# Kernel tuning notes

Hardware: AMD Instinct MI355X
Metric: run time of the kernel (lower is better)

## Reference

```python
import jax, jax.numpy as jnp
import numpy as np
from jax import lax

CHAOS_R = 3.5699456
N_STEPS = 10


def setup_inputs() -> dict:
    key = jax.random.key(0)
    k1, k2, k3 = jax.random.split(key, 3)
    B, T, D = 256, 8192, 5
    x = jax.random.normal(k1, (B, T, D), dtype=jnp.float32)
    temple = jax.random.normal(k2, (4, 5), dtype=jnp.float32)
    breath_vector = jax.random.normal(k3, (5,), dtype=jnp.float32)
    return {"x": x, "temple": temple, "breath_vector": breath_vector}


def reference(x, temple, breath_vector):
    # x: (B, T, D) with D == 5
    B, T, D = x.shape

    # mirror_sequence: chaos logistic map on mean of x[0,0]
    seed = jnp.mod(jnp.mean(x[0, 0]), 1.0)
    chaos = CHAOS_R * seed * (1.0 - seed)
    mirrored = jnp.where(chaos > 0.7, 9.0 - x,
                         jnp.where(chaos > 0.4, jnp.flip(x, axis=1), x))
    mode_code = jnp.where(chaos > 0.7, 0, jnp.where(chaos > 0.4, 1, 2))  # 0=invert,1=retrograde,2=none

    extended_x = jnp.concatenate([x, mirrored], axis=1)  # (B, 2T, D)

    # per-token breath: first T tokens use breath[:4], mirrored half uses breath[1:5]
    breath_main = breath_vector[:4]
    breath_mirror = breath_vector[1:5]
    breath = jnp.concatenate([
        jnp.broadcast_to(breath_main, (T, 4)),
        jnp.broadcast_to(breath_mirror, (T, 4)),
    ], axis=0)  # (2T, 4)

    def step(vec, _):
        # vec: (B, 2T, 5)
        transformed = jnp.einsum('rd,btd->btr', temple, vec)  # (B, 2T, 4)
        resonance = jnp.sum(transformed * breath[None, :, :], axis=-1)  # (B, 2T)
        vec = jnp.roll(vec, shift=1, axis=-1).at[..., 0].set(jnp.mod(resonance, 10.0))
        return vec, resonance

    vec0 = extended_x[..., :5]
    _, history = lax.scan(step, vec0, None, length=N_STEPS)  # (10, B, 2T)

    # torch.std default is unbiased (ddof=1)
    score = 1.0 / (1.0 + jnp.std(history, axis=0, ddof=1))  # (B, 2T)
    gate_weights = score[..., None]  # (B, 2T, 1)
    return gate_weights, extended_x, mode_code
```

## Files before the change

### kernel.cpp

```cpp
#include <hip/hip_runtime.h>

#define B_DIM 256
#define T_DIM 8192
#define D_DIM 5
#define NSTEPS 10

static constexpr long long GATE_N = (long long)B_DIM * (2 * T_DIM);
static constexpr long long EXT_N  = GATE_N * D_DIM;

__device__ __forceinline__ float scan_score(double v0, double v1, double v2, double v3, double v4,
                                            double w0, double w1, double w2, double w3, double w4) {
    float h[NSTEPS];
#pragma unroll
    for (int s = 0; s < NSTEPS; ++s) {
        double res = v0 * w0;
        res = fma(v1, w1, res);
        res = fma(v2, w2, res);
        res = fma(v3, w3, res);
        res = fma(v4, w4, res);
        h[s] = (float)res;
        double q = floor(res * 0.1);
        double m = fma(q, -10.0, res);
        m = (m < 0.0)   ? m + 10.0 : m;
        m = (m >= 10.0) ? m - 10.0 : m;
        v4 = v3; v3 = v2; v2 = v1; v1 = v0; v0 = m;
    }
    float mean = 0.f;
#pragma unroll
    for (int s = 0; s < NSTEPS; ++s) mean += h[s];
    mean *= 0.1f;
    float ssd = 0.f;
#pragma unroll
    for (int s = 0; s < NSTEPS; ++s) { float d = h[s] - mean; ssd = fmaf(d, d, ssd); }
    float sd = sqrtf(ssd * (1.0f / 9.0f));
    return 1.0f / (1.0f + sd);
}

__global__ __launch_bounds__(256) void temple_gate_kernel(
    const float* __restrict__ x, const float* __restrict__ temple,
    const float* __restrict__ breath, float* __restrict__ out) {
    __shared__ double sw[10];
    __shared__ int s_mode;

    if (threadIdx.x == 0) {
        double s = 0.0;
        for (int d = 0; d < 5; ++d) s += (double)x[d];
        s = s / 5.0;
        double seed = s - floor(s);
        double chaos = 3.5699456 * seed * (1.0 - seed);
        int mode = (chaos > 0.7) ? 0 : ((chaos > 0.4) ? 1 : 2);
        s_mode = mode;
        for (int d = 0; d < 5; ++d) {
            double wm = 0.0, wx = 0.0;
            for (int r = 0; r < 4; ++r) {
                double tv = (double)temple[r * 5 + d];
                wm += (double)breath[r] * tv;
                wx += (double)breath[r + 1] * tv;
            }
            sw[d] = wm; sw[5 + d] = wx;
        }
        if (blockIdx.x == 0) out[GATE_N + EXT_N] = (float)mode;
    }
    __syncthreads();

    const int mode = s_mode;
    const double wm0 = sw[0], wm1 = sw[1], wm2 = sw[2], wm3 = sw[3], wm4 = sw[4];
    const double wx0 = sw[5], wx1 = sw[6], wx2 = sw[7], wx3 = sw[8], wx4 = sw[9];

    const long long tid = (long long)blockIdx.x * blockDim.x + threadIdx.x;
    const int b = (int)(tid >> 13);
    const int t = (int)(tid & (T_DIM - 1));

    const float* xp = x + ((long long)b * T_DIM + t) * D_DIM;
    const float x0 = xp[0], x1 = xp[1], x2 = xp[2], x3 = xp[3], x4 = xp[4];

    float* gate = out;
    float* ext  = out + GATE_N;
    const long long rowBase = (long long)b * (2 * T_DIM);

    {
        const long long o = (rowBase + t) * D_DIM;
        ext[o + 0] = x0; ext[o + 1] = x1; ext[o + 2] = x2; ext[o + 3] = x3; ext[o + 4] = x4;
        gate[rowBase + t] = scan_score((double)x0, (double)x1, (double)x2, (double)x3, (double)x4,
                                       wm0, wm1, wm2, wm3, wm4);
    }

    {
        double m0 = (double)x0, m1 = (double)x1, m2 = (double)x2, m3 = (double)x3, m4 = (double)x4;
        float  f0 = x0, f1 = x1, f2 = x2, f3 = x3, f4 = x4;
        if (mode == 0) {
            m0 = 9.0 - m0; m1 = 9.0 - m1; m2 = 9.0 - m2; m3 = 9.0 - m3; m4 = 9.0 - m4;
            f0 = 9.f - x0; f1 = 9.f - x1; f2 = 9.f - x2; f3 = 9.f - x3; f4 = 9.f - x4;
        }
        const int tm = (mode == 1) ? (T_DIM - 1 - t) : t;
        const long long p = rowBase + T_DIM + tm;
        const long long o = p * D_DIM;
        ext[o + 0] = f0; ext[o + 1] = f1; ext[o + 2] = f2; ext[o + 3] = f3; ext[o + 4] = f4;
        gate[p] = scan_score(m0, m1, m2, m3, m4, wx0, wx1, wx2, wx3, wx4);
    }
}

extern "C" void kernel_launch(void* const* d_in, const int* in_sizes, int n_in,
                              void* d_out, int out_size, void* d_ws, size_t ws_size,
                              hipStream_t stream) {
    const float* x      = (const float*)d_in[0];
    const float* temple = (const float*)d_in[1];
    const float* breath = (const float*)d_in[2];
    float* out = (float*)d_out;

    const int total = B_DIM * T_DIM;
    temple_gate_kernel<<<total / 256, 256, 0, stream>>>(x, temple, breath, out);
}
```

Measured before the change: 145.1 us.

## Tile tokens through LDS with float4 coalesced loads and stores

Each block now handles a 1024-token tile. It loads the x tile with coalesced float4 reads into LDS, writes the extended output with float4 stores, and handles the retrograde case by reading the tile reversed from LDS. Each thread computes four tokens' scores and writes the gates as float4. The per-block mode and weight setup is now computed redundantly by every thread instead of once through shared memory. The aim is to replace the strided 5-float accesses with wide coalesced transfers, at the cost of fewer blocks and more work per thread.

After: 145.4 us. About the same (+0.2%).

```diff
diff --git a/kernel.cpp b/kernel.cpp
--- a/kernel.cpp
+++ b/kernel.cpp
@@ -1,23 +1,22 @@
 #include <hip/hip_runtime.h>
 
-#define B_DIM 256
-#define T_DIM 8192
-#define D_DIM 5
 #define NSTEPS 10
-
-static constexpr long long GATE_N = (long long)B_DIM * (2 * T_DIM);
-static constexpr long long EXT_N  = GATE_N * D_DIM;
+constexpr int B_DIM = 256, T_DIM = 8192, D_DIM = 5;
+constexpr int TILE  = 1024;
+constexpr int BLOCK = 256;
+constexpr long long GATE_N = (long long)B_DIM * 2 * T_DIM;
+constexpr long long EXT_N  = GATE_N * D_DIM;
 
 __device__ __forceinline__ float scan_score(double v0, double v1, double v2, double v3, double v4,
-                                            double w0, double w1, double w2, double w3, double w4) {
+                                            const double* __restrict__ w) {
     float h[NSTEPS];
 #pragma unroll
     for (int s = 0; s < NSTEPS; ++s) {
-        double res = v0 * w0;
-        res = fma(v1, w1, res);
-        res = fma(v2, w2, res);
-        res = fma(v3, w3, res);
-        res = fma(v4, w4, res);
+        double res = v0 * w[0];
+        res = fma(v1, w[1], res);
+        res = fma(v2, w[2], res);
+        res = fma(v3, w[3], res);
+        res = fma(v4, w[4], res);
         h[s] = (float)res;
         double q = floor(res * 0.1);
         double m = fma(q, -10.0, res);
@@ -36,67 +35,101 @@
     return 1.0f / (1.0f + sd);
 }
 
-__global__ __launch_bounds__(256) void temple_gate_kernel(
+__global__ __launch_bounds__(BLOCK) void temple_gate_kernel(
     const float* __restrict__ x, const float* __restrict__ temple,
     const float* __restrict__ breath, float* __restrict__ out) {
-    __shared__ double sw[10];
-    __shared__ int s_mode;
+    __shared__ float lds[TILE * D_DIM];
 
-    if (threadIdx.x == 0) {
-        double s = 0.0;
-        for (int d = 0; d < 5; ++d) s += (double)x[d];
-        s = s / 5.0;
-        double seed = s - floor(s);
-        double chaos = 3.5699456 * seed * (1.0 - seed);
-        int mode = (chaos > 0.7) ? 0 : ((chaos > 0.4) ? 1 : 2);
-        s_mode = mode;
-        for (int d = 0; d < 5; ++d) {
-            double wm = 0.0, wx = 0.0;
-            for (int r = 0; r < 4; ++r) {
-                double tv = (double)temple[r * 5 + d];
-                wm += (double)breath[r] * tv;
-                wx += (double)breath[r + 1] * tv;
-            }
-            sw[d] = wm; sw[5 + d] = wx;
+    const int k  = threadIdx.x;
+    const int b  = blockIdx.x >> 3;
+    const int t0 = (blockIdx.x & 7) * TILE;
+
+    double s = 0.0;
+    for (int d = 0; d < 5; ++d) s += (double)x[d];
+    s = s / 5.0;
+    double seed  = s - floor(s);
+    double chaos = 3.5699456 * seed * (1.0 - seed);
+    const int mode = (chaos > 0.7) ? 0 : ((chaos > 0.4) ? 1 : 2);
+    double wm[5], wx[5];
+#pragma unroll
+    for (int d = 0; d < 5; ++d) {
+        double a = 0.0, c = 0.0;
+#pragma unroll
+        for (int r = 0; r < 4; ++r) {
+            double tv = (double)temple[r * 5 + d];
+            a += (double)breath[r]     * tv;
+            c += (double)breath[r + 1] * tv;
         }
-        if (blockIdx.x == 0) out[GATE_N + EXT_N] = (float)mode;
+        wm[d] = a; wx[d] = c;
     }
-    __syncthreads();
+    if (blockIdx.x == 0 && k == 0) out[GATE_N + EXT_N] = (float)mode;
 
-    const int mode = s_mode;
-    const double wm0 = sw[0], wm1 = sw[1], wm2 = sw[2], wm3 = sw[3], wm4 = sw[4];
-    const double wx0 = sw[5], wx1 = sw[6], wx2 = sw[7], wx3 = sw[8], wx4 = sw[9];
+    const long long srcBase = ((long long)b * T_DIM + t0) * D_DIM;
+    const float4* __restrict__ src = (const float4*)(x + srcBase);
+    float4 r0 = src[k],       r1 = src[k + 256], r2 = src[k + 512],
+           r3 = src[k + 768], r4 = src[k + 1024];
 
-    const long long tid = (long long)blockIdx.x * blockDim.x + threadIdx.x;
-    const int b = (int)(tid >> 13);
-    const int t = (int)(tid & (T_DIM - 1));
-
-    const float* xp = x + ((long long)b * T_DIM + t) * D_DIM;
-    const float x0 = xp[0], x1 = xp[1], x2 = xp[2], x3 = xp[3], x4 = xp[4];
+    float4* l4 = (float4*)lds;
+    l4[k] = r0; l4[k + 256] = r1; l4[k + 512] = r2; l4[k + 768] = r3; l4[k + 1024] = r4;
 
     float* gate = out;
     float* ext  = out + GATE_N;
     const long long rowBase = (long long)b * (2 * T_DIM);
 
     {
-        const long long o = (rowBase + t) * D_DIM;
-        ext[o + 0] = x0; ext[o + 1] = x1; ext[o + 2] = x2; ext[o + 3] = x3; ext[o + 4] = x4;
-        gate[rowBase + t] = scan_score((double)x0, (double)x1, (double)x2, (double)x3, (double)x4,
-                                       wm0, wm1, wm2, wm3, wm4);
+        float4* dst = (float4*)(ext + (rowBase + t0) * D_DIM);
+        dst[k] = r0; dst[k + 256] = r1; dst[k + 512] = r2; dst[k + 768] = r3; dst[k + 1024] = r4;
+    }
+    if (mode == 0) {
+        float4* dst = (float4*)(ext + (rowBase + T_DIM + t0) * D_DIM);
+        float4 m0 = make_float4(9.f - r0.x, 9.f - r0.y, 9.f - r0.z, 9.f - r0.w);
+        float4 m1 = make_float4(9.f - r1.x, 9.f - r1.y, 9.f - r1.z, 9.f - r1.w);
+        float4 m2 = make_float4(9.f - r2.x, 9.f - r2.y, 9.f - r2.z, 9.f - r2.w);
+        float4 m3 = make_float4(9.f - r3.x, 9.f - r3.y, 9.f - r3.z, 9.f - r3.w);
+        float4 m4 = make_float4(9.f - r4.x, 9.f - r4.y, 9.f - r4.z, 9.f - r4.w);
+        dst[k] = m0; dst[k + 256] = m1; dst[k + 512] = m2; dst[k + 768] = m3; dst[k + 1024] = m4;
+    } else if (mode == 2) {
+        float4* dst = (float4*)(ext + (rowBase + T_DIM + t0) * D_DIM);
+        dst[k] = r0; dst[k + 256] = r1; dst[k + 512] = r2; dst[k + 768] = r3; dst[k + 1024] = r4;
+    }
+
+    __syncthreads();
+
+    if (mode == 1) {
+        float4* dst = (float4*)(ext + (rowBase + 2 * T_DIM - t0 - TILE) * D_DIM);
+#pragma unroll
+        for (int j = 0; j < 5; ++j) {
+            const int q = k + j * 256;
+            const int f = q * 4;
+            float v[4];
+#pragma unroll
+            for (int c = 0; c < 4; ++c) {
+                const int fc = f + c;
+                const int fi = fc / 5, d = fc - fi * 5;
+                v[c] = lds[(TILE - 1 - fi) * 5 + d];
+            }
+            dst[q] = make_float4(v[0], v[1], v[2], v[3]);
+        }
     }
 
     {
-        double m0 = (double)x0, m1 = (double)x1, m2 = (double)x2, m3 = (double)x3, m4 = (double)x4;
-        float  f0 = x0, f1 = x1, f2 = x2, f3 = x3, f4 = x4;
-        if (mode == 0) {
-            m0 = 9.0 - m0; m1 = 9.0 - m1; m2 = 9.0 - m2; m3 = 9.0 - m3; m4 = 9.0 - m4;
-            f0 = 9.f - x0; f1 = 9.f - x1; f2 = 9.f - x2; f3 = 9.f - x3; f4 = 9.f - x4;
+        const int itBase = 4 * k;
+        float gm[4], gx[4];
+#pragma unroll
+        for (int j = 0; j < 4; ++j) {
+            const float* p = &lds[(itBase + j) * 5];
+            double v0 = p[0], v1 = p[1], v2 = p[2], v3 = p[3], v4 = p[4];
+            gm[j] = scan_score(v0, v1, v2, v3, v4, wm);
+            if (mode == 0) { v0 = 9.0 - v0; v1 = 9.0 - v1; v2 = 9.0 - v2; v3 = 9.0 - v3; v4 = 9.0 - v4; }
+            gx[j] = scan_score(v0, v1, v2, v3, v4, wx);
         }
-        const int tm = (mode == 1) ? (T_DIM - 1 - t) : t;
-        const long long p = rowBase + T_DIM + tm;
-        const long long o = p * D_DIM;
-        ext[o + 0] = f0; ext[o + 1] = f1; ext[o + 2] = f2; ext[o + 3] = f3; ext[o + 4] = f4;
-        gate[p] = scan_score(m0, m1, m2, m3, m4, wx0, wx1, wx2, wx3, wx4);
+        ((float4*)(gate + rowBase + t0))[k] = make_float4(gm[0], gm[1], gm[2], gm[3]);
+        if (mode == 1) {
+            ((float4*)(gate + rowBase + 2 * T_DIM - t0 - TILE))[255 - k] =
+                make_float4(gx[3], gx[2], gx[1], gx[0]);
+        } else {
+            ((float4*)(gate + rowBase + T_DIM + t0))[k] = make_float4(gx[0], gx[1], gx[2], gx[3]);
+        }
     }
 }
 
@@ -108,6 +141,6 @@
     const float* breath = (const float*)d_in[2];
     float* out = (float*)d_out;
 
-    const int total = B_DIM * T_DIM;
-    temple_gate_kernel<<<total / 256, 256, 0, stream>>>(x, temple, breath, out);
+    const int blocks = (B_DIM * T_DIM) / TILE;
+    temple_gate_kernel<<<blocks, BLOCK, 0, stream>>>(x, temple, breath, out);
 }
```

## Split setup into separate kernel and vectorize extended-x copy with float4

Applied to the files above, without the earlier changes.

Moves the chaos-mode and weight precomputation into a single-thread setup kernel that writes to workspace, removing the per-block serial prologue and __syncthreads. The main kernel copies the contiguous 1280-float tile with coalesced float4 loads and stores for the main and non-retrograde mirrored halves, and interleaves the two independent scan chains for more ILP. Costs an extra kernel launch, a dependency on workspace, and a second uncoalesced read of x for the scalar scan inputs.

Result: no change. 143.1 us (-1.4%).

```diff
diff --git a/kernel.cpp b/kernel.cpp
--- a/kernel.cpp
+++ b/kernel.cpp
@@ -1,103 +1,109 @@
 #include <hip/hip_runtime.h>
 
-#define B_DIM 256
-#define T_DIM 8192
-#define D_DIM 5
-#define NSTEPS 10
+constexpr int B_DIM = 256, T_DIM = 8192;
+constexpr long long GATE_N = (long long)B_DIM * 2 * T_DIM;
+constexpr long long EXT_N  = GATE_N * 5;
 
-static constexpr long long GATE_N = (long long)B_DIM * (2 * T_DIM);
-static constexpr long long EXT_N  = GATE_N * D_DIM;
-
-__device__ __forceinline__ float scan_score(double v0, double v1, double v2, double v3, double v4,
-                                            double w0, double w1, double w2, double w3, double w4) {
-    float h[NSTEPS];
-#pragma unroll
-    for (int s = 0; s < NSTEPS; ++s) {
-        double res = v0 * w0;
-        res = fma(v1, w1, res);
-        res = fma(v2, w2, res);
-        res = fma(v3, w3, res);
-        res = fma(v4, w4, res);
-        h[s] = (float)res;
-        double q = floor(res * 0.1);
-        double m = fma(q, -10.0, res);
-        m = (m < 0.0)   ? m + 10.0 : m;
-        m = (m >= 10.0) ? m - 10.0 : m;
-        v4 = v3; v3 = v2; v2 = v1; v1 = v0; v0 = m;
+__global__ void temple_setup(const float* __restrict__ x, const float* __restrict__ temple,
+                             const float* __restrict__ breath,
+                             float* __restrict__ out, double* __restrict__ w) {
+    if (threadIdx.x != 0) return;
+    double s = 0.0;
+    for (int d = 0; d < 5; ++d) s += (double)x[d];
+    s = s / 5.0;
+    double seed  = s - floor(s);
+    double chaos = 3.5699456 * seed * (1.0 - seed);
+    int mode = (chaos > 0.7) ? 0 : ((chaos > 0.4) ? 1 : 2);
+    for (int d = 0; d < 5; ++d) {
+        double a = 0.0, c = 0.0;
+        for (int r = 0; r < 4; ++r) {
+            double tv = (double)temple[r * 5 + d];
+            a += (double)breath[r]     * tv;
+            c += (double)breath[r + 1] * tv;
+        }
+        w[d] = a; w[5 + d] = c;
     }
-    float mean = 0.f;
-#pragma unroll
-    for (int s = 0; s < NSTEPS; ++s) mean += h[s];
-    mean *= 0.1f;
-    float ssd = 0.f;
-#pragma unroll
-    for (int s = 0; s < NSTEPS; ++s) { float d = h[s] - mean; ssd = fmaf(d, d, ssd); }
-    float sd = sqrtf(ssd * (1.0f / 9.0f));
-    return 1.0f / (1.0f + sd);
+    w[10] = (double)mode;
+    out[GATE_N + EXT_N] = (float)mode;
 }
 
-__global__ __launch_bounds__(256) void temple_gate_kernel(
-    const float* __restrict__ x, const float* __restrict__ temple,
-    const float* __restrict__ breath, float* __restrict__ out) {
-    __shared__ double sw[10];
-    __shared__ int s_mode;
-
-    if (threadIdx.x == 0) {
-        double s = 0.0;
-        for (int d = 0; d < 5; ++d) s += (double)x[d];
-        s = s / 5.0;
-        double seed = s - floor(s);
-        double chaos = 3.5699456 * seed * (1.0 - seed);
-        int mode = (chaos > 0.7) ? 0 : ((chaos > 0.4) ? 1 : 2);
-        s_mode = mode;
-        for (int d = 0; d < 5; ++d) {
-            double wm = 0.0, wx = 0.0;
-            for (int r = 0; r < 4; ++r) {
-                double tv = (double)temple[r * 5 + d];
-                wm += (double)breath[r] * tv;
-                wx += (double)breath[r + 1] * tv;
-            }
-            sw[d] = wm; sw[5 + d] = wx;
-        }
-        if (blockIdx.x == 0) out[GATE_N + EXT_N] = (float)mode;
-    }
-    __syncthreads();
-
-    const int mode = s_mode;
-    const double wm0 = sw[0], wm1 = sw[1], wm2 = sw[2], wm3 = sw[3], wm4 = sw[4];
-    const double wx0 = sw[5], wx1 = sw[6], wx2 = sw[7], wx3 = sw[8], wx4 = sw[9];
-
-    const long long tid = (long long)blockIdx.x * blockDim.x + threadIdx.x;
-    const int b = (int)(tid >> 13);
-    const int t = (int)(tid & (T_DIM - 1));
-
-    const float* xp = x + ((long long)b * T_DIM + t) * D_DIM;
-    const float x0 = xp[0], x1 = xp[1], x2 = xp[2], x3 = xp[3], x4 = xp[4];
-
+__global__ __launch_bounds__(256) void temple_main(const float* __restrict__ x,
+                                                   const double* __restrict__ w,
+                                                   float* __restrict__ out) {
+    const int k  = threadIdx.x;
+    const int b  = blockIdx.x >> 5;
+    const int t0 = (blockIdx.x & 31) << 8;
+    const int mode = (int)w[10];
+    const long long rowBase = (long long)b * (2 * T_DIM);
     float* gate = out;
     float* ext  = out + GATE_N;
-    const long long rowBase = (long long)b * (2 * T_DIM);
 
-    {
-        const long long o = (rowBase + t) * D_DIM;
-        ext[o + 0] = x0; ext[o + 1] = x1; ext[o + 2] = x2; ext[o + 3] = x3; ext[o + 4] = x4;
-        gate[rowBase + t] = scan_score((double)x0, (double)x1, (double)x2, (double)x3, (double)x4,
-                                       wm0, wm1, wm2, wm3, wm4);
+    const float4* __restrict__ src4 = (const float4*)(x + ((long long)b * T_DIM + t0) * 5);
+    const bool extra = (k < 64);
+    float4 c0 = src4[k];
+    float4 c1;
+    if (extra) c1 = src4[256 + k];
+
+    float4* dmain = (float4*)(ext + (rowBase + t0) * 5);
+    dmain[k] = c0;
+    if (extra) dmain[256 + k] = c1;
+    if (mode == 0) {
+        float4* dmir = (float4*)(ext + (rowBase + T_DIM + t0) * 5);
+        dmir[k] = make_float4(9.f - c0.x, 9.f - c0.y, 9.f - c0.z, 9.f - c0.w);
+        if (extra) dmir[256 + k] = make_float4(9.f - c1.x, 9.f - c1.y, 9.f - c1.z, 9.f - c1.w);
+    } else if (mode == 2) {
+        float4* dmir = (float4*)(ext + (rowBase + T_DIM + t0) * 5);
+        dmir[k] = c0;
+        if (extra) dmir[256 + k] = c1;
     }
 
-    {
-        double m0 = (double)x0, m1 = (double)x1, m2 = (double)x2, m3 = (double)x3, m4 = (double)x4;
-        float  f0 = x0, f1 = x1, f2 = x2, f3 = x3, f4 = x4;
-        if (mode == 0) {
-            m0 = 9.0 - m0; m1 = 9.0 - m1; m2 = 9.0 - m2; m3 = 9.0 - m3; m4 = 9.0 - m4;
-            f0 = 9.f - x0; f1 = 9.f - x1; f2 = 9.f - x2; f3 = 9.f - x3; f4 = 9.f - x4;
-        }
-        const int tm = (mode == 1) ? (T_DIM - 1 - t) : t;
-        const long long p = rowBase + T_DIM + tm;
-        const long long o = p * D_DIM;
-        ext[o + 0] = f0; ext[o + 1] = f1; ext[o + 2] = f2; ext[o + 3] = f3; ext[o + 4] = f4;
-        gate[p] = scan_score(m0, m1, m2, m3, m4, wx0, wx1, wx2, wx3, wx4);
+    const int t = t0 + k;
+    const float* __restrict__ xi = x + ((long long)b * T_DIM + t) * 5;
+    const float x0 = xi[0], x1 = xi[1], x2 = xi[2], x3 = xi[3], x4 = xi[4];
+
+    if (mode == 1) {
+        float* dm = ext + (rowBase + 2 * T_DIM - 1 - t) * 5;
+        dm[0] = x0; dm[1] = x1; dm[2] = x2; dm[3] = x3; dm[4] = x4;
     }
+
+    const double wa0 = w[0], wa1 = w[1], wa2 = w[2], wa3 = w[3], wa4 = w[4];
+    const double wb0 = w[5], wb1 = w[6], wb2 = w[7], wb3 = w[8], wb4 = w[9];
+    double a0 = x0, a1 = x1, a2 = x2, a3 = x3, a4 = x4;
+    double b0, b1, b2, b3, b4;
+    if (mode == 0) { b0 = 9.0 - a0; b1 = 9.0 - a1; b2 = 9.0 - a2; b3 = 9.0 - a3; b4 = 9.0 - a4; }
+    else           { b0 = a0; b1 = a1; b2 = a2; b3 = a3; b4 = a4; }
+
+    float ha[10], hb[10];
+#pragma unroll
+    for (int s = 0; s < 10; ++s) {
+        double ra = a0 * wa0;
+        ra = fma(a1, wa1, ra); ra = fma(a2, wa2, ra); ra = fma(a3, wa3, ra); ra = fma(a4, wa4, ra);
+        double rb = b0 * wb0;
+        rb = fma(b1, wb1, rb); rb = fma(b2, wb2, rb); rb = fma(b3, wb3, rb); rb = fma(b4, wb4, rb);
+        ha[s] = (float)ra; hb[s] = (float)rb;
+        double qa = floor(ra * 0.1), ma = fma(qa, -10.0, ra);
+        ma = (ma < 0.0) ? ma + 10.0 : ma;  ma = (ma >= 10.0) ? ma - 10.0 : ma;
+        double qb = floor(rb * 0.1), mb = fma(qb, -10.0, rb);
+        mb = (mb < 0.0) ? mb + 10.0 : mb;  mb = (mb >= 10.0) ? mb - 10.0 : mb;
+        a4 = a3; a3 = a2; a2 = a1; a1 = a0; a0 = ma;
+        b4 = b3; b3 = b2; b2 = b1; b1 = b0; b0 = mb;
+    }
+    float meanA = 0.f, meanB = 0.f;
+#pragma unroll
+    for (int s = 0; s < 10; ++s) { meanA += ha[s]; meanB += hb[s]; }
+    meanA *= 0.1f; meanB *= 0.1f;
+    float ssdA = 0.f, ssdB = 0.f;
+#pragma unroll
+    for (int s = 0; s < 10; ++s) {
+        float da = ha[s] - meanA; ssdA = fmaf(da, da, ssdA);
+        float db = hb[s] - meanB; ssdB = fmaf(db, db, ssdB);
+    }
+    const float gm = 1.0f / (1.0f + sqrtf(ssdA * (1.0f / 9.0f)));
+    const float gx = 1.0f / (1.0f + sqrtf(ssdB * (1.0f / 9.0f)));
+
+    gate[rowBase + t] = gm;
+    if (mode == 1) gate[rowBase + 2 * T_DIM - 1 - t] = gx;
+    else           gate[rowBase + T_DIM + t] = gx;
 }
 
 extern "C" void kernel_launch(void* const* d_in, const int* in_sizes, int n_in,
@@ -107,7 +113,9 @@
     const float* temple = (const float*)d_in[1];
     const float* breath = (const float*)d_in[2];
     float* out = (float*)d_out;
+    double* w  = (double*)d_ws;
 
-    const int total = B_DIM * T_DIM;
-    temple_gate_kernel<<<total / 256, 256, 0, stream>>>(x, temple, breath, out);
+    temple_setup<<<1, 64, 0, stream>>>(x, temple, breath, out, w);
+    const int blocks = (B_DIM * T_DIM) / 256;
+    temple_main<<<blocks, 256, 0, stream>>>(x, w, out);
 }
```
